# Performance work log

Measured on AMD Instinct MI355X. Metric: run time of the kernel, lower is better.

The kernel has to match this reference:

```python
import jax, jax.numpy as jnp
import numpy as np

D_MODEL = 1024
NHEAD = 16
HEAD_DIM = D_MODEL // NHEAD
HIDDEN = 4 * D_MODEL  # SwiGLU hidden_dim
B, L = 2, 2048
EPS = 1e-8


def _alibi_slopes(n):
    # standard ALiBi slopes: geometric sequence 2^(-8/n * i)
    return np.array([2 ** (-8.0 / n * (i + 1)) for i in range(n)], dtype=np.float32)


def setup_inputs() -> dict:
    key = jax.random.key(0)
    ks = jax.random.split(key, 10)
    x = jax.random.normal(ks[0], (B, L, D_MODEL), dtype=jnp.float32)
    # causal mask: True where attention is disallowed (j > i)
    attn_mask = jnp.triu(jnp.ones((L, L), dtype=bool), k=1)[None, None]
    # ALiBi bias: -slope * (i - j) for j <= i; value on masked positions irrelevant
    pos = jnp.arange(L)
    dist = (pos[:, None] - pos[None, :]).astype(jnp.float32)  # [L,L]
    slopes = jnp.asarray(_alibi_slopes(NHEAD))
    alibi_bias = (-slopes[:, None, None] * dist)[None]  # [1,H,L,L]
    s = 0.02
    w_qkv = jax.random.normal(ks[1], (D_MODEL, 3 * D_MODEL), dtype=jnp.float32) * s
    b_qkv = jnp.zeros((3 * D_MODEL,), jnp.float32)
    w_o = jax.random.normal(ks[2], (D_MODEL, D_MODEL), dtype=jnp.float32) * s
    b_o = jnp.zeros((D_MODEL,), jnp.float32)
    scale1 = jnp.ones((D_MODEL,), jnp.float32)
    scale2 = jnp.ones((D_MODEL,), jnp.float32)
    w1 = jax.random.normal(ks[3], (D_MODEL, 2 * HIDDEN), dtype=jnp.float32) * s
    b1 = jnp.zeros((2 * HIDDEN,), jnp.float32)
    w2 = jax.random.normal(ks[4], (HIDDEN, D_MODEL), dtype=jnp.float32) * s
    b2 = jnp.zeros((D_MODEL,), jnp.float32)
    return dict(x=x, attn_mask=attn_mask, alibi_bias=alibi_bias,
                w_qkv=w_qkv, b_qkv=b_qkv, w_o=w_o, b_o=b_o,
                scale1=scale1, scale2=scale2, w1=w1, b1=b1, w2=w2, b2=b2)


def rmsnorm(x, scale):
    return scale * (x * jax.lax.rsqrt(jnp.mean(x * x, axis=-1, keepdims=True) + EPS))


def reference(x, attn_mask, alibi_bias, w_qkv, b_qkv, w_o, b_o,
              scale1, scale2, w1, b1, w2, b2):
    Bv, Lv, D = x.shape
    xn = rmsnorm(x, scale1)
    qkv = xn @ w_qkv + b_qkv  # [B,L,3D]
    q, k, v = jnp.split(qkv, 3, axis=-1)
    def to_heads(t):
        return t.reshape(Bv, Lv, NHEAD, HEAD_DIM).transpose(0, 2, 1, 3)  # [B,H,L,Dh]
    q, k, v = to_heads(q), to_heads(k), to_heads(v)
    scores = jnp.einsum('bhqd,bhkd->bhqk', q, k) / (HEAD_DIM ** 0.5)
    scores = scores + alibi_bias[:, :, :Lv, :Lv]
    scores = jnp.where(attn_mask, -jnp.inf, scores)
    attn = jax.nn.softmax(scores, axis=-1)
    out = jnp.einsum('bhqk,bhkd->bhqd', attn, v)  # [B,H,L,Dh]
    out = out.transpose(0, 2, 1, 3).reshape(Bv, Lv, D)
    x = x + (out @ w_o + b_o)
    # SwiGLU FFN
    h = rmsnorm(x, scale2) @ w1 + b1
    x_proj, gate = jnp.split(h, 2, axis=-1)
    ffn = (jax.nn.silu(gate) * x_proj) @ w2 + b2
    return x + ffn
```

## Files before the change

### kernel.cpp

```cpp
#include <hip/hip_runtime.h>
#include <hip/hip_bf16.h>
#include <stdint.h>

typedef __hip_bfloat16 bf16;
typedef __bf16 bf16x8 __attribute__((ext_vector_type(8)));
typedef float f32x4 __attribute__((ext_vector_type(4)));

#define DM   1024
#define LSEQ 2048
#define NH   16
#define DH   64
#define BB   2
#define HID  4096
#define MROWS (BB*LSEQ)

__device__ __forceinline__ void load_lds16(const void* g, void* l) {
    __builtin_amdgcn_global_load_lds(
        (const __attribute__((address_space(1))) unsigned int*)g,
        (__attribute__((address_space(3))) unsigned int*)l, 16, 0, 0);
}

__global__ void transpose_cast_f32_bf16(const float* __restrict__ src,
                                        bf16* __restrict__ dst, int R, int C) {
    __shared__ float tile[32][33];
    const int c0 = blockIdx.x * 32, r0 = blockIdx.y * 32;
    const int tx = threadIdx.x & 31, ty = threadIdx.x >> 5;
#pragma unroll
    for (int i = 0; i < 32; i += 8)
        tile[ty + i][tx] = src[(size_t)(r0 + ty + i) * C + c0 + tx];
    __syncthreads();
#pragma unroll
    for (int i = 0; i < 32; i += 8)
        dst[(size_t)(c0 + ty + i) * R + r0 + tx] = __float2bfloat16(tile[tx][ty + i]);
}

__global__ void transpose_bf16_batched(const bf16* __restrict__ src,
                                       bf16* __restrict__ dst, int R, int C) {
    const size_t zoff = (size_t)blockIdx.z * R * C;
    src += zoff; dst += zoff;
    __shared__ bf16 tile[32][33];
    const int c0 = blockIdx.x * 32, r0 = blockIdx.y * 32;
    const int tx = threadIdx.x & 31, ty = threadIdx.x >> 5;
#pragma unroll
    for (int i = 0; i < 32; i += 8)
        tile[ty + i][tx] = src[(size_t)(r0 + ty + i) * C + c0 + tx];
    __syncthreads();
#pragma unroll
    for (int i = 0; i < 32; i += 8)
        dst[(size_t)(c0 + ty + i) * R + r0 + tx] = tile[tx][ty + i];
}

__global__ __launch_bounds__(256)
void rmsnorm_cast(const float* __restrict__ x, const float* __restrict__ scale,
                  bf16* __restrict__ out) {
    const int row = blockIdx.x;
    const int tid = threadIdx.x;
    const float4 v = ((const float4*)(x + (size_t)row * DM))[tid];
    float ss = v.x * v.x + v.y * v.y + v.z * v.z + v.w * v.w;
#pragma unroll
    for (int off = 32; off >= 1; off >>= 1) ss += __shfl_xor(ss, off);
    __shared__ float part[4];
    if ((tid & 63) == 0) part[tid >> 6] = ss;
    __syncthreads();
    const float tot = part[0] + part[1] + part[2] + part[3];
    const float rs = rsqrtf(tot * (1.0f / DM) + 1e-8f);
    const float4 s = ((const float4*)scale)[tid];
    union { bf16 h[4]; uint2 u; } pk;
    pk.h[0] = __float2bfloat16(v.x * rs * s.x);
    pk.h[1] = __float2bfloat16(v.y * rs * s.y);
    pk.h[2] = __float2bfloat16(v.z * rs * s.z);
    pk.h[3] = __float2bfloat16(v.w * rs * s.w);
    ((uint2*)(out + (size_t)row * DM))[tid] = pk.u;
}

template <typename Epi>
__global__ __launch_bounds__(256, 2)
void gemm_bt(const bf16* __restrict__ A, const bf16* __restrict__ Bt,
             int M, int N, int K, Epi epi) {
    __shared__ __align__(16) bf16 sA[128 * 32];
    __shared__ __align__(16) bf16 sB[128 * 32];
    const int tid = threadIdx.x;
    const int wave = tid >> 6, lane = tid & 63;
    const int lo = lane & 15, hi = lane >> 4;
    const int wm = wave & 1, wn = wave >> 1;
    const int m0 = blockIdx.x * 128, n0 = blockIdx.y * 128;
    const int rowA = lane >> 2, cc = (lane & 3) * 8;

    f32x4 acc[4][4];
#pragma unroll
    for (int i = 0; i < 4; i++)
#pragma unroll
        for (int j = 0; j < 4; j++) acc[i][j] = (f32x4){0.f, 0.f, 0.f, 0.f};

    const int nk = K >> 5;
    for (int kt = 0; kt < nk; ++kt) {
        const int k0 = kt * 32;
#pragma unroll
        for (int i = 0; i < 2; ++i) {
            const int slot = wave * 2 + i;
            load_lds16(A + (size_t)(m0 + slot * 16 + rowA) * K + k0 + cc, &sA[slot * 512]);
            load_lds16(Bt + (size_t)(n0 + slot * 16 + rowA) * K + k0 + cc, &sB[slot * 512]);
        }
        __syncthreads();
        bf16x8 a[4], b[4];
#pragma unroll
        for (int i = 0; i < 4; i++)
            a[i] = *(const bf16x8*)&sA[(wm * 64 + i * 16 + lo) * 32 + hi * 8];
#pragma unroll
        for (int j = 0; j < 4; j++)
            b[j] = *(const bf16x8*)&sB[(wn * 64 + j * 16 + lo) * 32 + hi * 8];
#pragma unroll
        for (int i = 0; i < 4; i++)
#pragma unroll
            for (int j = 0; j < 4; j++)
                acc[i][j] = __builtin_amdgcn_mfma_f32_16x16x32_bf16(a[i], b[j], acc[i][j], 0, 0, 0);
        __syncthreads();
    }
#pragma unroll
    for (int i = 0; i < 4; i++) {
        const int row = m0 + wm * 64 + i * 16 + hi * 4;
#pragma unroll
        for (int j = 0; j < 4; j++) {
            const int col = n0 + wn * 64 + j * 16 + lo;
#pragma unroll
            for (int r = 0; r < 4; r++) epi(row + r, col, acc[i][j][r]);
        }
    }
}

struct EpiQKV {
    const float* bias; bf16* q; bf16* k; bf16* v;
    __device__ void operator()(int row, int col, float val) const {
        const float r = val + bias[col];
        const int which = col >> 10, rem = col & 1023;
        const int h = rem >> 6, d = rem & 63;
        const int b = row >> 11, l = row & 2047;
        bf16* dst = which == 0 ? q : (which == 1 ? k : v);
        dst[(((size_t)(b * NH + h)) * LSEQ + l) * DH + d] = __float2bfloat16(r);
    }
};
struct EpiBiasResidF32 {
    const float* bias; const float* res; float* out; int ldc;
    __device__ void operator()(int row, int col, float val) const {
        const size_t idx = (size_t)row * ldc + col;
        out[idx] = val + bias[col] + res[idx];
    }
};
struct EpiBiasBF16 {
    const float* bias; bf16* out; int ldc;
    __device__ void operator()(int row, int col, float val) const {
        out[(size_t)row * ldc + col] = __float2bfloat16(val + bias[col]);
    }
};

__global__ __launch_bounds__(256, 2)
void attn_flash(const bf16* __restrict__ Q, const bf16* __restrict__ Kg,
                const bf16* __restrict__ Vt, bf16* __restrict__ O) {
    const int bh = blockIdx.x, qt = blockIdx.y;
    const int b = bh >> 4, h = bh & 15;
    const int tid = threadIdx.x, wave = tid >> 6, lane = tid & 63;
    const int lo = lane & 15, hi = lane >> 4;
    __shared__ __align__(16) bf16 sQ[64 * 64];
    __shared__ __align__(16) bf16 sK[64 * 64];
    __shared__ __align__(16) bf16 sV[64 * 64];
    __shared__ __align__(16) bf16 sP[4][16 * 64];

    const float slope = exp2f(-0.5f * (float)(h + 1));
    const float LOG2E = 1.44269504088896340736f;
    const int q0 = qt * 64;
    const bf16* Qb = Q + (size_t)bh * LSEQ * DH;
    const bf16* Kb = Kg + (size_t)bh * LSEQ * DH;
    const bf16* Vb = Vt + (size_t)bh * DH * LSEQ;

#pragma unroll
    for (int i = 0; i < 2; ++i) {
        const int s = wave * 2 + i;
        load_lds16(Qb + (size_t)(q0 + s * 8 + (lane >> 3)) * DH + (lane & 7) * 8, &sQ[s * 512]);
    }
    __syncthreads();
    bf16x8 aq0 = *(const bf16x8*)&sQ[(wave * 16 + lo) * 64 + hi * 8];
    bf16x8 aq1 = *(const bf16x8*)&sQ[(wave * 16 + lo) * 64 + 32 + hi * 8];

    f32x4 accO[4];
#pragma unroll
    for (int j = 0; j < 4; j++) accO[j] = (f32x4){0.f, 0.f, 0.f, 0.f};
    float mrun[4], lrun[4];
#pragma unroll
    for (int r = 0; r < 4; r++) { mrun[r] = -3.0e30f; lrun[r] = 0.f; }
    const int irow0 = q0 + wave * 16 + hi * 4;

    for (int kt = 0; kt <= qt; ++kt) {
        __syncthreads();
#pragma unroll
        for (int i = 0; i < 2; ++i) {
            const int s = wave * 2 + i;
            load_lds16(Kb + (size_t)(kt * 64 + s * 8 + (lane >> 3)) * DH + (lane & 7) * 8, &sK[s * 512]);
            load_lds16(Vb + (size_t)(s * 8 + (lane >> 3)) * LSEQ + kt * 64 + (lane & 7) * 8, &sV[s * 512]);
        }
        __syncthreads();

        f32x4 s4[4];
#pragma unroll
        for (int j = 0; j < 4; j++) {
            bf16x8 bk0 = *(const bf16x8*)&sK[(j * 16 + lo) * 64 + hi * 8];
            bf16x8 bk1 = *(const bf16x8*)&sK[(j * 16 + lo) * 64 + 32 + hi * 8];
            f32x4 z = (f32x4){0.f, 0.f, 0.f, 0.f};
            z = __builtin_amdgcn_mfma_f32_16x16x32_bf16(aq0, bk0, z, 0, 0, 0);
            z = __builtin_amdgcn_mfma_f32_16x16x32_bf16(aq1, bk1, z, 0, 0, 0);
            s4[j] = z;
        }
        float p[4][4], mx[4];
#pragma unroll
        for (int r = 0; r < 4; r++) mx[r] = -3.0e30f;
#pragma unroll
        for (int j = 0; j < 4; j++) {
            const int jg = kt * 64 + j * 16 + lo;
#pragma unroll
            for (int r = 0; r < 4; r++) {
                const int ig = irow0 + r;
                float val = (jg > ig) ? -3.0e30f
                          : (s4[j][r] * 0.125f - slope * (float)(ig - jg)) * LOG2E;
                p[j][r] = val;
                mx[r] = fmaxf(mx[r], val);
            }
        }
#pragma unroll
        for (int off = 8; off >= 1; off >>= 1)
#pragma unroll
            for (int r = 0; r < 4; r++) mx[r] = fmaxf(mx[r], __shfl_xor(mx[r], off));
        float alpha[4], rssum[4];
#pragma unroll
        for (int r = 0; r < 4; r++) {
            const float mnew = fmaxf(mrun[r], mx[r]);
            alpha[r] = exp2f(mrun[r] - mnew);
            mrun[r] = mnew;
            rssum[r] = 0.f;
        }
#pragma unroll
        for (int j = 0; j < 4; j++)
#pragma unroll
            for (int r = 0; r < 4; r++) {
                const float pv = exp2f(p[j][r] - mrun[r]);
                p[j][r] = pv;
                rssum[r] += pv;
            }
#pragma unroll
        for (int off = 8; off >= 1; off >>= 1)
#pragma unroll
            for (int r = 0; r < 4; r++) rssum[r] += __shfl_xor(rssum[r], off);
#pragma unroll
        for (int r = 0; r < 4; r++) lrun[r] = lrun[r] * alpha[r] + rssum[r];
#pragma unroll
        for (int j = 0; j < 4; j++)
#pragma unroll
            for (int r = 0; r < 4; r++) accO[j][r] *= alpha[r];
#pragma unroll
        for (int j = 0; j < 4; j++)
#pragma unroll
            for (int r = 0; r < 4; r++)
                sP[wave][(hi * 4 + r) * 64 + j * 16 + lo] = __float2bfloat16(p[j][r]);
        bf16x8 ap0 = *(const bf16x8*)&sP[wave][lo * 64 + hi * 8];
        bf16x8 ap1 = *(const bf16x8*)&sP[wave][lo * 64 + 32 + hi * 8];
#pragma unroll
        for (int j = 0; j < 4; j++) {
            bf16x8 bv0 = *(const bf16x8*)&sV[(j * 16 + lo) * 64 + hi * 8];
            bf16x8 bv1 = *(const bf16x8*)&sV[(j * 16 + lo) * 64 + 32 + hi * 8];
            accO[j] = __builtin_amdgcn_mfma_f32_16x16x32_bf16(ap0, bv0, accO[j], 0, 0, 0);
            accO[j] = __builtin_amdgcn_mfma_f32_16x16x32_bf16(ap1, bv1, accO[j], 0, 0, 0);
        }
    }
    bf16* Ob = O + (size_t)b * LSEQ * DM + (size_t)h * DH;
#pragma unroll
    for (int r = 0; r < 4; r++) {
        const float inv = 1.0f / lrun[r];
        const int row = q0 + wave * 16 + hi * 4 + r;
#pragma unroll
        for (int j = 0; j < 4; j++)
            Ob[(size_t)row * DM + j * 16 + lo] = __float2bfloat16(accO[j][r] * inv);
    }
}

__global__ __launch_bounds__(256)
void swiglu_kernel(const bf16* __restrict__ h, bf16* __restrict__ out) {
    const size_t e = ((size_t)blockIdx.x * 256 + threadIdx.x) * 8;
    const int r = (int)(e >> 12), c = (int)(e & 4095);
    const bf16x8 xv = *(const bf16x8*)(h + (size_t)r * (2 * HID) + c);
    const bf16x8 gv = *(const bf16x8*)(h + (size_t)r * (2 * HID) + HID + c);
    bf16x8 o;
#pragma unroll
    for (int t = 0; t < 8; t++) {
        const float g = (float)gv[t];
        const float s = g / (1.f + __expf(-g));
        o[t] = (__bf16)(s * (float)xv[t]);
    }
    *(bf16x8*)(out + (size_t)r * HID + c) = o;
}

extern "C" void kernel_launch(void* const* d_in, const int* in_sizes, int n_in,
                              void* d_out, int out_size, void* d_ws, size_t ws_size,
                              hipStream_t stream) {
    const float* x      = (const float*)d_in[0];
    const float* w_qkv  = (const float*)d_in[3];
    const float* b_qkv  = (const float*)d_in[4];
    const float* w_o    = (const float*)d_in[5];
    const float* b_o    = (const float*)d_in[6];
    const float* scale1 = (const float*)d_in[7];
    const float* scale2 = (const float*)d_in[8];
    const float* w1     = (const float*)d_in[9];
    const float* b1     = (const float*)d_in[10];
    const float* w2     = (const float*)d_in[11];
    const float* b2     = (const float*)d_in[12];
    float* out = (float*)d_out;

    uint8_t* w = (uint8_t*)d_ws;
    size_t off = 0;
    auto take = [&](size_t bytes) { void* p = w + off; off += (bytes + 255) & ~(size_t)255; return p; };
    bf16* xn    = (bf16*)take((size_t)MROWS * DM * 2);
    bf16* wqkvT = (bf16*)take((size_t)3 * DM * DM * 2);
    bf16* woT   = (bf16*)take((size_t)DM * DM * 2);
    bf16* w1T   = (bf16*)take((size_t)2 * HID * DM * 2);
    bf16* w2T   = (bf16*)take((size_t)DM * HID * 2);
    bf16* qb    = (bf16*)take((size_t)MROWS * DM * 2);
    bf16* kb    = (bf16*)take((size_t)MROWS * DM * 2);
    bf16* vb    = (bf16*)take((size_t)MROWS * DM * 2);
    bf16* vt    = (bf16*)take((size_t)MROWS * DM * 2);
    bf16* ao    = (bf16*)take((size_t)MROWS * DM * 2);
    float* x1   = (float*)take((size_t)MROWS * DM * 4);
    bf16* xn2   = (bf16*)take((size_t)MROWS * DM * 2);
    bf16* hbuf  = (bf16*)take((size_t)MROWS * 2 * HID * 2);
    bf16* ffn   = (bf16*)take((size_t)MROWS * HID * 2);

    transpose_cast_f32_bf16<<<dim3(3 * DM / 32, DM / 32), 256, 0, stream>>>(w_qkv, wqkvT, DM, 3 * DM);
    transpose_cast_f32_bf16<<<dim3(DM / 32, DM / 32), 256, 0, stream>>>(w_o, woT, DM, DM);
    transpose_cast_f32_bf16<<<dim3(2 * HID / 32, DM / 32), 256, 0, stream>>>(w1, w1T, DM, 2 * HID);
    transpose_cast_f32_bf16<<<dim3(DM / 32, HID / 32), 256, 0, stream>>>(w2, w2T, HID, DM);

    rmsnorm_cast<<<MROWS, 256, 0, stream>>>(x, scale1, xn);

    EpiQKV e1{b_qkv, qb, kb, vb};
    gemm_bt<EpiQKV><<<dim3(MROWS / 128, 3 * DM / 128), 256, 0, stream>>>(xn, wqkvT, MROWS, 3 * DM, DM, e1);

    transpose_bf16_batched<<<dim3(DH / 32, LSEQ / 32, BB * NH), 256, 0, stream>>>(vb, vt, LSEQ, DH);

    attn_flash<<<dim3(BB * NH, LSEQ / 64), 256, 0, stream>>>(qb, kb, vt, ao);

    EpiBiasResidF32 e2{b_o, x, x1, DM};
    gemm_bt<EpiBiasResidF32><<<dim3(MROWS / 128, DM / 128), 256, 0, stream>>>(ao, woT, MROWS, DM, DM, e2);

    rmsnorm_cast<<<MROWS, 256, 0, stream>>>(x1, scale2, xn2);

    EpiBiasBF16 e3{b1, hbuf, 2 * HID};
    gemm_bt<EpiBiasBF16><<<dim3(MROWS / 128, 2 * HID / 128), 256, 0, stream>>>(xn2, w1T, MROWS, 2 * HID, DM, e3);

    swiglu_kernel<<<(int)(((size_t)MROWS * HID / 8) / 256), 256, 0, stream>>>(hbuf, ffn);

    EpiBiasResidF32 e4{b2, x1, out, DM};
    gemm_bt<EpiBiasResidF32><<<dim3(MROWS / 128, DM / 128), 256, 0, stream>>>(ffn, w2T, MROWS, DM, HID, e4);
}
```

Baseline: 757.5 us.

## Fuse SwiGLU into FFN1 GEMM epilogue and keep QKV in row-major layout

The w1 columns are interleaved during the weight transpose so that each x_proj/gate pair sits in adjacent output columns. The SwiGLU activation is then computed in the FFN1 GEMM epilogue with a lane shuffle, which removes the separate swiglu kernel and the large intermediate hidden buffer round trip through memory. The QKV GEMM now writes one contiguous row-major buffer, and attention reads Q and K from it with a strided layout. The four weight-transpose launches are merged into one. In exchange, only half the lanes do stores in the SwiGLU epilogue, and Q/K loads in attention use a wider row stride.

```diff
diff --git a/kernel.cpp b/kernel.cpp
--- a/kernel.cpp
+++ b/kernel.cpp
@@ -13,6 +13,7 @@
 #define BB   2
 #define HID  4096
 #define MROWS (BB*LSEQ)
+#define QLD  (3*DM)
 
 __device__ __forceinline__ void load_lds16(const void* g, void* l) {
     __builtin_amdgcn_global_load_lds(
@@ -20,34 +21,45 @@
         (__attribute__((address_space(3))) unsigned int*)l, 16, 0, 0);
 }
 
-__global__ void transpose_cast_f32_bf16(const float* __restrict__ src,
-                                        bf16* __restrict__ dst, int R, int C) {
+__global__ __launch_bounds__(256)
+void transpose_all(const float* __restrict__ wqkv, const float* __restrict__ wo,
+                   const float* __restrict__ w1, const float* __restrict__ w2,
+                   bf16* __restrict__ wqkvT, bf16* __restrict__ woT,
+                   bf16* __restrict__ w1T, bf16* __restrict__ w2T) {
+    int bid = blockIdx.x;
+    const float* src; bf16* dst; int R, C, bx, by; bool inter = false;
+    if (bid < 3072)       { src = wqkv; dst = wqkvT; R = 1024; C = 3072; bx = bid % 96;  by = bid / 96; }
+    else if (bid < 4096)  { bid -= 3072;  src = wo; dst = woT;  R = 1024; C = 1024; bx = bid % 32;  by = bid / 32; }
+    else if (bid < 12288) { bid -= 4096;  src = w1; dst = w1T;  R = 1024; C = 8192; bx = bid % 256; by = bid / 256; inter = true; }
+    else                  { bid -= 12288; src = w2; dst = w2T;  R = 4096; C = 1024; bx = bid % 32;  by = bid / 32; }
     __shared__ float tile[32][33];
-    const int c0 = blockIdx.x * 32, r0 = blockIdx.y * 32;
+    const int c0 = bx * 32, r0 = by * 32;
     const int tx = threadIdx.x & 31, ty = threadIdx.x >> 5;
 #pragma unroll
     for (int i = 0; i < 32; i += 8)
         tile[ty + i][tx] = src[(size_t)(r0 + ty + i) * C + c0 + tx];
     __syncthreads();
 #pragma unroll
+    for (int i = 0; i < 32; i += 8) {
+        const int c = c0 + ty + i;
+        const int drow = inter ? ((c < HID) ? 2 * c : 2 * (c - HID) + 1) : c;
+        dst[(size_t)drow * R + r0 + tx] = __float2bfloat16(tile[tx][ty + i]);
+    }
+}
+
+__global__ __launch_bounds__(256)
+void v_transpose(const bf16* __restrict__ qkv, bf16* __restrict__ vt) {
+    const int bh = blockIdx.z, b = bh >> 4, h = bh & 15;
+    const int l0 = blockIdx.x * 32, d0 = blockIdx.y * 32;
+    __shared__ bf16 tile[32][33];
+    const int tx = threadIdx.x & 31, ty = threadIdx.x >> 5;
+#pragma unroll
     for (int i = 0; i < 32; i += 8)
-        dst[(size_t)(c0 + ty + i) * R + r0 + tx] = __float2bfloat16(tile[tx][ty + i]);
-}
-
-__global__ void transpose_bf16_batched(const bf16* __restrict__ src,
-                                       bf16* __restrict__ dst, int R, int C) {
-    const size_t zoff = (size_t)blockIdx.z * R * C;
-    src += zoff; dst += zoff;
-    __shared__ bf16 tile[32][33];
-    const int c0 = blockIdx.x * 32, r0 = blockIdx.y * 32;
-    const int tx = threadIdx.x & 31, ty = threadIdx.x >> 5;
+        tile[ty + i][tx] = qkv[((size_t)b * LSEQ + l0 + ty + i) * QLD + 2 * DM + h * DH + d0 + tx];
+    __syncthreads();
 #pragma unroll
     for (int i = 0; i < 32; i += 8)
-        tile[ty + i][tx] = src[(size_t)(r0 + ty + i) * C + c0 + tx];
-    __syncthreads();
-#pragma unroll
-    for (int i = 0; i < 32; i += 8)
-        dst[(size_t)(c0 + ty + i) * R + r0 + tx] = tile[tx][ty + i];
+        vt[((size_t)bh * DH + d0 + ty + i) * LSEQ + l0 + tx] = tile[tx][ty + i];
 }
 
 __global__ __launch_bounds__(256)
@@ -128,15 +140,10 @@
     }
 }
 
-struct EpiQKV {
-    const float* bias; bf16* q; bf16* k; bf16* v;
+struct EpiBiasBF16 {
+    const float* bias; bf16* out; int ldc;
     __device__ void operator()(int row, int col, float val) const {
-        const float r = val + bias[col];
-        const int which = col >> 10, rem = col & 1023;
-        const int h = rem >> 6, d = rem & 63;
-        const int b = row >> 11, l = row & 2047;
-        bf16* dst = which == 0 ? q : (which == 1 ? k : v);
-        dst[(((size_t)(b * NH + h)) * LSEQ + l) * DH + d] = __float2bfloat16(r);
+        out[(size_t)row * ldc + col] = __float2bfloat16(val + bias[col]);
     }
 };
 struct EpiBiasResidF32 {
@@ -146,16 +153,22 @@
         out[idx] = val + bias[col] + res[idx];
     }
 };
-struct EpiBiasBF16 {
-    const float* bias; bf16* out; int ldc;
+struct EpiSwiGLU {
+    const float* b1; bf16* out;
     __device__ void operator()(int row, int col, float val) const {
-        out[(size_t)row * ldc + col] = __float2bfloat16(val + bias[col]);
+        const int orig = (col >> 1) + ((col & 1) ? HID : 0);
+        const float v = val + b1[orig];
+        const float other = __shfl_xor(v, 1);
+        const float g = other;
+        const float s = g / (1.f + __expf(-g));
+        if (!(threadIdx.x & 1))
+            out[(size_t)row * HID + (col >> 1)] = __float2bfloat16(s * v);
     }
 };
 
 __global__ __launch_bounds__(256, 2)
-void attn_flash(const bf16* __restrict__ Q, const bf16* __restrict__ Kg,
-                const bf16* __restrict__ Vt, bf16* __restrict__ O) {
+void attn_flash(const bf16* __restrict__ qkv, const bf16* __restrict__ Vt,
+                bf16* __restrict__ O) {
     const int bh = blockIdx.x, qt = blockIdx.y;
     const int b = bh >> 4, h = bh & 15;
     const int tid = threadIdx.x, wave = tid >> 6, lane = tid & 63;
@@ -168,14 +181,14 @@
     const float slope = exp2f(-0.5f * (float)(h + 1));
     const float LOG2E = 1.44269504088896340736f;
     const int q0 = qt * 64;
-    const bf16* Qb = Q + (size_t)bh * LSEQ * DH;
-    const bf16* Kb = Kg + (size_t)bh * LSEQ * DH;
+    const bf16* Qb = qkv + (size_t)b * LSEQ * QLD + h * DH;
+    const bf16* Kb = Qb + DM;
     const bf16* Vb = Vt + (size_t)bh * DH * LSEQ;
 
 #pragma unroll
     for (int i = 0; i < 2; ++i) {
         const int s = wave * 2 + i;
-        load_lds16(Qb + (size_t)(q0 + s * 8 + (lane >> 3)) * DH + (lane & 7) * 8, &sQ[s * 512]);
+        load_lds16(Qb + (size_t)(q0 + s * 8 + (lane >> 3)) * QLD + (lane & 7) * 8, &sQ[s * 512]);
     }
     __syncthreads();
     bf16x8 aq0 = *(const bf16x8*)&sQ[(wave * 16 + lo) * 64 + hi * 8];
@@ -194,7 +207,7 @@
 #pragma unroll
         for (int i = 0; i < 2; ++i) {
             const int s = wave * 2 + i;
-            load_lds16(Kb + (size_t)(kt * 64 + s * 8 + (lane >> 3)) * DH + (lane & 7) * 8, &sK[s * 512]);
+            load_lds16(Kb + (size_t)(kt * 64 + s * 8 + (lane >> 3)) * QLD + (lane & 7) * 8, &sK[s * 512]);
             load_lds16(Vb + (size_t)(s * 8 + (lane >> 3)) * LSEQ + kt * 64 + (lane & 7) * 8, &sV[s * 512]);
         }
         __syncthreads();
@@ -278,22 +291,6 @@
         for (int j = 0; j < 4; j++)
             Ob[(size_t)row * DM + j * 16 + lo] = __float2bfloat16(accO[j][r] * inv);
     }
-}
-
-__global__ __launch_bounds__(256)
-void swiglu_kernel(const bf16* __restrict__ h, bf16* __restrict__ out) {
-    const size_t e = ((size_t)blockIdx.x * 256 + threadIdx.x) * 8;
-    const int r = (int)(e >> 12), c = (int)(e & 4095);
-    const bf16x8 xv = *(const bf16x8*)(h + (size_t)r * (2 * HID) + c);
-    const bf16x8 gv = *(const bf16x8*)(h + (size_t)r * (2 * HID) + HID + c);
-    bf16x8 o;
-#pragma unroll
-    for (int t = 0; t < 8; t++) {
-        const float g = (float)gv[t];
-        const float s = g / (1.f + __expf(-g));
-        o[t] = (__bf16)(s * (float)xv[t]);
-    }
-    *(bf16x8*)(out + (size_t)r * HID + c) = o;
 }
 
 extern "C" void kernel_launch(void* const* d_in, const int* in_sizes, int n_in,
@@ -320,39 +317,31 @@
     bf16* woT   = (bf16*)take((size_t)DM * DM * 2);
     bf16* w1T   = (bf16*)take((size_t)2 * HID * DM * 2);
     bf16* w2T   = (bf16*)take((size_t)DM * HID * 2);
-    bf16* qb    = (bf16*)take((size_t)MROWS * DM * 2);
-    bf16* kb    = (bf16*)take((size_t)MROWS * DM * 2);
-    bf16* vb    = (bf16*)take((size_t)MROWS * DM * 2);
+    bf16* qkvb  = (bf16*)take((size_t)MROWS * QLD * 2);
     bf16* vt    = (bf16*)take((size_t)MROWS * DM * 2);
     bf16* ao    = (bf16*)take((size_t)MROWS * DM * 2);
     float* x1   = (float*)take((size_t)MROWS * DM * 4);
     bf16* xn2   = (bf16*)take((size_t)MROWS * DM * 2);
-    bf16* hbuf  = (bf16*)take((size_t)MROWS * 2 * HID * 2);
     bf16* ffn   = (bf16*)take((size_t)MROWS * HID * 2);
 
-    transpose_cast_f32_bf16<<<dim3(3 * DM / 32, DM / 32), 256, 0, stream>>>(w_qkv, wqkvT, DM, 3 * DM);
-    transpose_cast_f32_bf16<<<dim3(DM / 32, DM / 32), 256, 0, stream>>>(w_o, woT, DM, DM);
-    transpose_cast_f32_bf16<<<dim3(2 * HID / 32, DM / 32), 256, 0, stream>>>(w1, w1T, DM, 2 * HID);
-    transpose_cast_f32_bf16<<<dim3(DM / 32, HID / 32), 256, 0, stream>>>(w2, w2T, HID, DM);
+    transpose_all<<<16384, 256, 0, stream>>>(w_qkv, w_o, w1, w2, wqkvT, woT, w1T, w2T);
 
     rmsnorm_cast<<<MROWS, 256, 0, stream>>>(x, scale1, xn);
 
-    EpiQKV e1{b_qkv, qb, kb, vb};
-    gemm_bt<EpiQKV><<<dim3(MROWS / 128, 3 * DM / 128), 256, 0, stream>>>(xn, wqkvT, MROWS, 3 * DM, DM, e1);
-
-    transpose_bf16_batched<<<dim3(DH / 32, LSEQ / 32, BB * NH), 256, 0, stream>>>(vb, vt, LSEQ, DH);
-
-    attn_flash<<<dim3(BB * NH, LSEQ / 64), 256, 0, stream>>>(qb, kb, vt, ao);
+    EpiBiasBF16 e1{b_qkv, qkvb, QLD};
+    gemm_bt<EpiBiasBF16><<<dim3(MROWS / 128, QLD / 128), 256, 0, stream>>>(xn, wqkvT, MROWS, QLD, DM, e1);
+
+    v_transpose<<<dim3(LSEQ / 32, DH / 32, BB * NH), 256, 0, stream>>>(qkvb, vt);
+
+    attn_flash<<<dim3(BB * NH, LSEQ / 64), 256, 0, stream>>>(qkvb, vt, ao);
 
     EpiBiasResidF32 e2{b_o, x, x1, DM};
     gemm_bt<EpiBiasResidF32><<<dim3(MROWS / 128, DM / 128), 256, 0, stream>>>(ao, woT, MROWS, DM, DM, e2);
 
     rmsnorm_cast<<<MROWS, 256, 0, stream>>>(x1, scale2, xn2);
 
-    EpiBiasBF16 e3{b1, hbuf, 2 * HID};
-    gemm_bt<EpiBiasBF16><<<dim3(MROWS / 128, 2 * HID / 128), 256, 0, stream>>>(xn2, w1T, MROWS, 2 * HID, DM, e3);
-
-    swiglu_kernel<<<(int)(((size_t)MROWS * HID / 8) / 256), 256, 0, stream>>>(hbuf, ffn);
+    EpiSwiGLU e3{b1, ffn};
+    gemm_bt<EpiSwiGLU><<<dim3(MROWS / 128, 2 * HID / 128), 256, 0, stream>>>(xn2, w1T, MROWS, 2 * HID, DM, e3);
 
     EpiBiasResidF32 e4{b2, x1, out, DM};
     gemm_bt<EpiBiasResidF32><<<dim3(MROWS / 128, DM / 128), 256, 0, stream>>>(ffn, w2T, MROWS, DM, HID, e4);
```

Result: faster. 742.2 us (-2.0%).
